# Kernel optimization log

Measured on AMD Instinct MI355X. Metric: run time of the kernel, lower is better.

The kernel has to match this reference:

```python
import jax, jax.numpy as jnp
import numpy as np
import math

B, S, D, H = 2, 2048, 2048, 16
HD = D // H            # 128
FF = 4 * D             # 8192
EPS = 1e-5


def _alibi_slopes(num_heads):
    # power-of-2 path (16 heads): slopes = base^i, base = 2^(-2^-(log2(n)-3))
    closest = 2 ** math.floor(math.log2(num_heads))
    base = 2.0 ** (-(2.0 ** (-(math.log2(closest) - 3))))
    powers = np.arange(1, 1 + closest, dtype=np.float32)
    slopes = base ** powers
    if closest != num_heads:
        extra_base = 2.0 ** (-(2.0 ** (-(math.log2(2 * closest) - 3))))
        num_rem = min(closest, num_heads - closest)
        extra_powers = np.arange(1, 1 + 2 * num_rem, 2, dtype=np.float32)
        slopes = np.concatenate([slopes, extra_base ** extra_powers])
    return jnp.asarray(slopes, dtype=jnp.float32)


def setup_inputs() -> dict:
    key = jax.random.key(0)
    ks = jax.random.split(key, 8)
    s = 0.02
    return {
        "x": jax.random.normal(ks[0], (B, S, D), dtype=jnp.float32),
        "ln1_w": jnp.ones((D,), jnp.float32),
        "ln1_b": jnp.zeros((D,), jnp.float32),
        "wqkv": jax.random.normal(ks[1], (D, 3 * D), jnp.float32) * s,
        "bqkv": jnp.zeros((3 * D,), jnp.float32),
        "wo": jax.random.normal(ks[2], (D, D), jnp.float32) * s,
        "bo": jnp.zeros((D,), jnp.float32),
        "ln2_w": jnp.ones((D,), jnp.float32),
        "ln2_b": jnp.zeros((D,), jnp.float32),
        "w1": jax.random.normal(ks[3], (D, FF), jnp.float32) * s,
        "b1": jnp.zeros((FF,), jnp.float32),
        "w2": jax.random.normal(ks[4], (FF, D), jnp.float32) * s,
        "b2": jnp.zeros((D,), jnp.float32),
    }


def _ln(x, w, b):
    mu = jnp.mean(x, axis=-1, keepdims=True)
    var = jnp.mean(jnp.square(x - mu), axis=-1, keepdims=True)
    return (x - mu) * jax.lax.rsqrt(var + EPS) * w + b


def reference(x, ln1_w, ln1_b, wqkv, bqkv, wo, bo, ln2_w, ln2_b, w1, b1, w2, b2):
    slopes = _alibi_slopes(H)                      # [H]
    # --- input layernorm + attention ---
    h = _ln(x, ln1_w, ln1_b)
    qkv = h @ wqkv + bqkv                          # [B,S,3D]
    q, k, v = jnp.split(qkv, 3, axis=-1)
    q = q.reshape(B, S, H, HD).transpose(0, 2, 1, 3)  # [B,H,S,HD]
    k = k.reshape(B, S, H, HD).transpose(0, 2, 1, 3)
    v = v.reshape(B, S, H, HD).transpose(0, 2, 1, 3)
    scores = jnp.einsum("bhqd,bhkd->bhqk", q, k) / math.sqrt(HD)
    pos = jnp.arange(S, dtype=jnp.float32)
    rel = pos[None, :] - pos[:, None]              # j - i
    alibi = slopes[:, None, None] * rel[None]      # [H,S,S]
    scores = scores.astype(jnp.float32) + alibi[None]
    causal = rel <= 0                              # j <= i
    scores = jnp.where(causal[None, None], scores, jnp.finfo(jnp.float32).min)
    probs = jax.nn.softmax(scores, axis=-1).astype(x.dtype)
    attn = jnp.einsum("bhqk,bhkd->bhqd", probs, v)  # [B,H,S,HD]
    attn = attn.transpose(0, 2, 1, 3).reshape(B, S, D)
    x = x + attn @ wo + bo
    # --- post-attn layernorm + GELU MLP ---
    h2 = _ln(x, ln2_w, ln2_b)
    m = jax.nn.gelu(h2 @ w1 + b1, approximate=True) @ w2 + b2
    return x + m
```

## Files before the change

kernel.cpp:

```cpp
#include <hip/hip_runtime.h>
#include <hip/hip_bf16.h>
#include <stdint.h>

#define BB 2
#define SS 2048
#define DD 2048
#define HH 16
#define HD 128
#define FFD 8192
#define TD (3*DD)

typedef unsigned short u16;
typedef __attribute__((ext_vector_type(8))) short s16x8;
typedef __attribute__((ext_vector_type(4))) float f32x4;

struct alignas(8) U16x4 { u16 a, b, c, d; };

__device__ __forceinline__ u16 f2b(float f) {
  union { float f; uint32_t u; } v; v.f = f;
  uint32_t r = (v.u + 0x7fffu + ((v.u >> 16) & 1u)) >> 16;
  return (u16)r;
}

__device__ __forceinline__ void async16(const void* g, void* l) {
  __builtin_amdgcn_global_load_lds((const __attribute__((address_space(1))) void*)g,
                                   (__attribute__((address_space(3))) void*)l,
                                   16, 0, 0);
}

__global__ __launch_bounds__(256) void wconv_t(const float* __restrict__ W,
                                               u16* __restrict__ Wt, int K, int N) {
  __shared__ float tile[64][65];
  int k0 = blockIdx.x * 64, n0 = blockIdx.y * 64;
  int c = threadIdx.x & 63, r0 = threadIdx.x >> 6;
#pragma unroll
  for (int i = 0; i < 16; ++i) {
    int r = i * 4 + r0;
    tile[r][c] = W[(size_t)(k0 + r) * N + n0 + c];
  }
  __syncthreads();
#pragma unroll
  for (int i = 0; i < 16; ++i) {
    int n = i * 4 + r0;
    Wt[(size_t)(n0 + n) * K + k0 + c] = f2b(tile[c][n]);
  }
}

__global__ __launch_bounds__(256) void ln_kernel(const float* __restrict__ X,
                                                 const float* __restrict__ g,
                                                 const float* __restrict__ be,
                                                 u16* __restrict__ O) {
  int row = blockIdx.x;
  const float* xr = X + (size_t)row * DD;
  int t = threadIdx.x;
  float4 v0 = ((const float4*)xr)[t];
  float4 v1 = ((const float4*)xr)[t + 256];
  float s = v0.x + v0.y + v0.z + v0.w + v1.x + v1.y + v1.z + v1.w;
  float q = v0.x*v0.x + v0.y*v0.y + v0.z*v0.z + v0.w*v0.w
          + v1.x*v1.x + v1.y*v1.y + v1.z*v1.z + v1.w*v1.w;
#pragma unroll
  for (int o = 32; o > 0; o >>= 1) { s += __shfl_down(s, o); q += __shfl_down(q, o); }
  __shared__ float red[8];
  if ((t & 63) == 0) { red[t >> 6] = s; red[4 + (t >> 6)] = q; }
  __syncthreads();
  float S = red[0] + red[1] + red[2] + red[3];
  float Q = red[4] + red[5] + red[6] + red[7];
  float mu = S * (1.0f / DD);
  float var = Q * (1.0f / DD) - mu * mu;
  float rs = rsqrtf(var + 1e-5f);
  float4 g0 = ((const float4*)g)[t],  g1 = ((const float4*)g)[t + 256];
  float4 b0 = ((const float4*)be)[t], b1 = ((const float4*)be)[t + 256];
  U16x4 o0, o1;
  o0.a = f2b((v0.x - mu) * rs * g0.x + b0.x);
  o0.b = f2b((v0.y - mu) * rs * g0.y + b0.y);
  o0.c = f2b((v0.z - mu) * rs * g0.z + b0.z);
  o0.d = f2b((v0.w - mu) * rs * g0.w + b0.w);
  o1.a = f2b((v1.x - mu) * rs * g1.x + b1.x);
  o1.b = f2b((v1.y - mu) * rs * g1.y + b1.y);
  o1.c = f2b((v1.z - mu) * rs * g1.z + b1.z);
  o1.d = f2b((v1.w - mu) * rs * g1.w + b1.w);
  *(U16x4*)(O + (size_t)row * DD + t * 4)         = o0;
  *(U16x4*)(O + (size_t)row * DD + (t + 256) * 4) = o1;
}

template <int MODE>
__global__ __launch_bounds__(256) void gemm_bt(const u16* __restrict__ A,
                                               const u16* __restrict__ Bt,
                                               const float* __restrict__ bias,
                                               const float* __restrict__ res,
                                               void* __restrict__ Cout,
                                               int M, int N, int K) {
  __shared__ __align__(16) u16 As[128 * 64];
  __shared__ __align__(16) u16 Bs[128 * 64];
  int n0 = blockIdx.x * 128, m0 = blockIdx.y * 128;
  int tid = threadIdx.x;
  int lane = tid & 63, w = tid >> 6;
  int wm = w >> 1, wn = w & 1;
  int col = lane & 15, quad = lane >> 4;
  f32x4 acc[4][4] = {};
  int arow = tid >> 3;
  int gkb = (tid & 7) ^ (arow & 7);
  const u16* ag = A  + (size_t)(m0 + arow) * K + gkb * 8;
  const u16* bg = Bt + (size_t)(n0 + arow) * K + gkb * 8;
  int sw = col & 7;
  for (int k0 = 0; k0 < K; k0 += 64) {
    __syncthreads();
#pragma unroll
    for (int s = 0; s < 4; ++s) {
      async16(ag + (size_t)s * 32 * K + k0, &As[s * 2048 + tid * 8]);
      async16(bg + (size_t)s * 32 * K + k0, &Bs[s * 2048 + tid * 8]);
    }
    __syncthreads();
#pragma unroll
    for (int kk = 0; kk < 64; kk += 32) {
      int kb = (kk >> 3) + quad;
      int slot = (kb ^ sw) * 8;
      s16x8 af[4], bf[4];
#pragma unroll
      for (int mt = 0; mt < 4; ++mt)
        af[mt] = *(const s16x8*)&As[(wm * 64 + mt * 16 + col) * 64 + slot];
#pragma unroll
      for (int nt = 0; nt < 4; ++nt)
        bf[nt] = *(const s16x8*)&Bs[(wn * 64 + nt * 16 + col) * 64 + slot];
#pragma unroll
      for (int mt = 0; mt < 4; ++mt)
#pragma unroll
        for (int nt = 0; nt < 4; ++nt)
          acc[mt][nt] = __builtin_amdgcn_mfma_f32_16x16x32_bf16(af[mt], bf[nt], acc[mt][nt], 0, 0, 0);
    }
  }
#pragma unroll
  for (int mt = 0; mt < 4; ++mt) {
    int mg = m0 + wm * 64 + mt * 16 + quad * 4;
#pragma unroll
    for (int nt = 0; nt < 4; ++nt) {
      int ng = n0 + wn * 64 + nt * 16 + col;
      float bn = bias[ng];
#pragma unroll
      for (int r = 0; r < 4; ++r) {
        float v = acc[mt][nt][r] + bn;
        size_t idx = (size_t)(mg + r) * N + ng;
        if (MODE == 1) {
          float u = 1.5957691216057308f * (v + 0.044715f * v * v * v);
          v = v / (1.0f + __expf(-u));
        }
        if (MODE == 2) {
          ((float*)Cout)[idx] = v + res[idx];
        } else {
          ((u16*)Cout)[idx] = f2b(v);
        }
      }
    }
  }
}

__global__ __launch_bounds__(256) void attn_kernel(const u16* __restrict__ qkv,
                                                   u16* __restrict__ out) {
  __shared__ __align__(16) u16 Ks[2][64 * 128];
  __shared__ __align__(16) u16 Vts[128 * 64];
  __shared__ __align__(16) u16 Ps[4][16 * 72];
  int bx = blockIdx.x, h = blockIdx.y, b = blockIdx.z;
  int tid = threadIdx.x, lane = tid & 63, w = tid >> 6;
  int col = lane & 15, quad = lane >> 4;
  const u16* base  = qkv + (size_t)b * SS * TD + (size_t)h * HD;
  const u16* kbase = base + DD;
  const u16* vbase = base + 2 * DD;
  float slope = exp2f(-0.5f * (float)(h + 1));
  const float scale = 0.088388347648318447f;
  int krow = tid >> 4;
  int ghb = (tid & 15) ^ (krow & 7);
  int vkey_loc = tid >> 4;
  int vhd0 = (tid & 15) * 8;
  int kxc = 8 * (tid & 7);

#pragma unroll 1
  for (int ph = 0; ph < 2; ++ph) {
    int qt = ph ? (31 - bx) : bx;
    int q0 = qt * 64;
    int ntile = qt + 1;
    int qr = q0 + w * 16 + col;
    s16x8 qf[4];
#pragma unroll
    for (int c = 0; c < 4; ++c)
      qf[c] = *(const s16x8*)(base + (size_t)qr * TD + c * 32 + quad * 8);
    float m_i[4] = {-1e30f, -1e30f, -1e30f, -1e30f};
    float l_i[4] = {0.f, 0.f, 0.f, 0.f};
    f32x4 oacc[8] = {};
#pragma unroll
    for (int s = 0; s < 4; ++s)
      async16(kbase + (size_t)(s * 16 + krow) * TD + ghb * 8,
              &Ks[0][s * 2048 + tid * 8]);
    s16x8 vreg[4];
#pragma unroll
    for (int s = 0; s < 4; ++s)
      vreg[s] = *(const s16x8*)(vbase + (size_t)(s * 16 + vkey_loc) * TD + vhd0);

    for (int t = 0; t < ntile; ++t) {
      int j0 = t * 64;
      __syncthreads();
      if (t + 1 < ntile) {
#pragma unroll
        for (int s = 0; s < 4; ++s)
          async16(kbase + (size_t)(j0 + 64 + s * 16 + krow) * TD + ghb * 8,
                  &Ks[(t + 1) & 1][s * 2048 + tid * 8]);
      }
#pragma unroll
      for (int s = 0; s < 4; ++s) {
        int key = s * 16 + vkey_loc;
#pragma unroll
        for (int j = 0; j < 8; ++j)
          Vts[(vhd0 + j) * 64 + (key ^ kxc)] = (u16)vreg[s][j];
      }
      if (t + 1 < ntile) {
#pragma unroll
        for (int s = 0; s < 4; ++s)
          vreg[s] = *(const s16x8*)(vbase + (size_t)(j0 + 64 + s * 16 + vkey_loc) * TD + vhd0);
      }
      const u16* kt_ = Ks[t & 1];
      f32x4 sc[4];
#pragma unroll
      for (int nt = 0; nt < 4; ++nt) {
        f32x4 s4 = {0.f, 0.f, 0.f, 0.f};
        int key = nt * 16 + col;
        int ksw = col & 7;
#pragma unroll
        for (int c = 0; c < 4; ++c) {
          s16x8 kf = *(const s16x8*)&kt_[key * 128 + (((c * 4 + quad) ^ ksw) * 8)];
          s4 = __builtin_amdgcn_mfma_f32_16x16x32_bf16(qf[c], kf, s4, 0, 0, 0);
        }
        sc[nt] = s4;
      }
      int rb = q0 + w * 16 + quad * 4;
      float p[4][4];
      float mt_[4] = {-1e30f, -1e30f, -1e30f, -1e30f};
#pragma unroll
      for (int nt = 0; nt < 4; ++nt) {
        int j = j0 + nt * 16 + col;
#pragma unroll
        for (int r = 0; r < 4; ++r) {
          float v = sc[nt][r] * scale + slope * (float)(j - (rb + r));
          if (j > rb + r) v = -1e30f;
          p[nt][r] = v;
          mt_[r] = fmaxf(mt_[r], v);
        }
      }
#pragma unroll
      for (int o = 1; o < 16; o <<= 1)
#pragma unroll
        for (int r = 0; r < 4; ++r) mt_[r] = fmaxf(mt_[r], __shfl_xor(mt_[r], o));
      float alpha[4];
#pragma unroll
      for (int r = 0; r < 4; ++r) {
        float mn = fmaxf(m_i[r], mt_[r]);
        alpha[r] = __expf(m_i[r] - mn);
        m_i[r] = mn;
      }
      float ls[4] = {0.f, 0.f, 0.f, 0.f};
#pragma unroll
      for (int nt = 0; nt < 4; ++nt)
#pragma unroll
        for (int r = 0; r < 4; ++r) {
          float e = __expf(p[nt][r] - m_i[r]);
          p[nt][r] = e;
          ls[r] += e;
        }
#pragma unroll
      for (int o = 1; o < 16; o <<= 1)
#pragma unroll
        for (int r = 0; r < 4; ++r) ls[r] += __shfl_xor(ls[r], o);
#pragma unroll
      for (int r = 0; r < 4; ++r) l_i[r] = l_i[r] * alpha[r] + ls[r];
#pragma unroll
      for (int ot = 0; ot < 8; ++ot)
#pragma unroll
        for (int r = 0; r < 4; ++r) oacc[ot][r] *= alpha[r];
#pragma unroll
      for (int nt = 0; nt < 4; ++nt)
#pragma unroll
        for (int r = 0; r < 4; ++r)
          Ps[w][(quad * 4 + r) * 72 + nt * 16 + col] = f2b(p[nt][r]);
      __syncthreads();
#pragma unroll
      for (int kt = 0; kt < 2; ++kt) {
        s16x8 pf = *(const s16x8*)&Ps[w][col * 72 + kt * 32 + quad * 8];
        int k8 = kt * 32 + quad * 8;
#pragma unroll
        for (int ot = 0; ot < 8; ++ot) {
          int hd = ot * 16 + col;
          int swz = 8 * ((hd >> 3) & 7);
          s16x8 vf = *(const s16x8*)&Vts[hd * 64 + (k8 ^ swz)];
          oacc[ot] = __builtin_amdgcn_mfma_f32_16x16x32_bf16(pf, vf, oacc[ot], 0, 0, 0);
        }
      }
    }
#pragma unroll
    for (int r = 0; r < 4; ++r) l_i[r] = 1.0f / l_i[r];
    u16* ob = out + ((size_t)b * SS + q0 + w * 16 + quad * 4) * DD + h * HD;
#pragma unroll
    for (int ot = 0; ot < 8; ++ot)
#pragma unroll
      for (int r = 0; r < 4; ++r)
        ob[(size_t)r * DD + ot * 16 + col] = f2b(oacc[ot][r] * l_i[r]);
  }
}

extern "C" void kernel_launch(void* const* d_in, const int* in_sizes, int n_in,
                              void* d_out, int out_size, void* d_ws, size_t ws_size,
                              hipStream_t stream) {
  const float* x    = (const float*)d_in[0];
  const float* ln1w = (const float*)d_in[1];
  const float* ln1b = (const float*)d_in[2];
  const float* wqkv = (const float*)d_in[3];
  const float* bqkv = (const float*)d_in[4];
  const float* wo   = (const float*)d_in[5];
  const float* bo   = (const float*)d_in[6];
  const float* ln2w = (const float*)d_in[7];
  const float* ln2b = (const float*)d_in[8];
  const float* w1   = (const float*)d_in[9];
  const float* b1   = (const float*)d_in[10];
  const float* w2   = (const float*)d_in[11];
  const float* b2   = (const float*)d_in[12];

  const int M = BB * SS;
  char* ws = (char*)d_ws;
  u16*  wt   = (u16*)ws;
  u16*  qkv  = (u16*)(ws + 33554432ull);
  u16*  cbuf = (u16*)(ws + 33554432ull + 50331648ull);
  float* r1  = (float*)(ws + 33554432ull + 50331648ull + 67108864ull);
  u16* h1 = cbuf;
  u16* attn = cbuf;
  u16* m1 = cbuf;
  u16* h2 = qkv;

  ln_kernel<<<M, 256, 0, stream>>>(x, ln1w, ln1b, h1);
  wconv_t<<<dim3(DD / 64, TD / 64), 256, 0, stream>>>(wqkv, wt, DD, TD);
  gemm_bt<0><<<dim3(TD / 128, M / 128), 256, 0, stream>>>(h1, wt, bqkv, nullptr, qkv, M, TD, DD);
  attn_kernel<<<dim3(16, HH, BB), 256, 0, stream>>>(qkv, attn);
  wconv_t<<<dim3(DD / 64, DD / 64), 256, 0, stream>>>(wo, wt, DD, DD);
  gemm_bt<2><<<dim3(DD / 128, M / 128), 256, 0, stream>>>(attn, wt, bo, x, r1, M, DD, DD);
  ln_kernel<<<M, 256, 0, stream>>>(r1, ln2w, ln2b, h2);
  wconv_t<<<dim3(DD / 64, FFD / 64), 256, 0, stream>>>(w1, wt, DD, FFD);
  gemm_bt<1><<<dim3(FFD / 128, M / 128), 256, 0, stream>>>(h2, wt, b1, nullptr, m1, M, FFD, DD);
  wconv_t<<<dim3(FFD / 64, DD / 64), 256, 0, stream>>>(w2, wt, FFD, DD);
  gemm_bt<2><<<dim3(DD / 128, M / 128), 256, 0, stream>>>(m1, wt, b2, r1, (float*)d_out, M, DD, FFD);
}
```

Measured before the change: 885.0 us.

## Replace GEMM with 8-wave 256x128 double-buffered pipelined kernel

The bf16 GEMM is replaced by an 8-wave (512-thread) kernel that computes a 256x128 output tile per block. Operand tiles are double-buffered in LDS, with the next K-tile's async loads issued while MFMAs run on the current buffer, and explicit vmcnt waits and s_barrier replace the two __syncthreads per iteration. It also uses s_setprio around the MFMA block and a new LDS swizzle for 32-wide K halves. The aim is to hide global-load latency and raise MFMA utilisation, at the cost of more LDS (two buffers) and fewer blocks in the grid.

```diff
diff --git a/kernel.cpp b/kernel.cpp
--- a/kernel.cpp
+++ b/kernel.cpp
@@ -84,51 +84,79 @@
 }
 
 template <int MODE>
-__global__ __launch_bounds__(256) void gemm_bt(const u16* __restrict__ A,
-                                               const u16* __restrict__ Bt,
-                                               const float* __restrict__ bias,
-                                               const float* __restrict__ res,
-                                               void* __restrict__ Cout,
-                                               int M, int N, int K) {
-  __shared__ __align__(16) u16 As[128 * 64];
-  __shared__ __align__(16) u16 Bs[128 * 64];
-  int n0 = blockIdx.x * 128, m0 = blockIdx.y * 128;
+__global__ __launch_bounds__(512, 2) void gemm8(const u16* __restrict__ A,
+                                                const u16* __restrict__ Bt,
+                                                const float* __restrict__ bias,
+                                                const float* __restrict__ res,
+                                                void* __restrict__ Cout,
+                                                int M, int N, int K) {
+  __shared__ __align__(16) u16 As[2][2][256 * 32];
+  __shared__ __align__(16) u16 Bs[2][2][128 * 32];
+
+  int n0 = blockIdx.x * 128, m0 = blockIdx.y * 256;
   int tid = threadIdx.x;
   int lane = tid & 63, w = tid >> 6;
-  int wm = w >> 1, wn = w & 1;
+  int wn = w & 1, wm = w >> 1;
   int col = lane & 15, quad = lane >> 4;
+
+  int r = tid >> 2, sl = tid & 3;
+  int gks = (sl ^ ((r >> 1) & 3)) * 8;
+  const u16* ag = A  + (size_t)(m0 + r) * K + gks;
+  const u16* bg = Bt + (size_t)(n0 + r) * K + gks;
+
+  int swz = (col >> 1) & 3;
+  int aoff = (wm * 64) * 32 + col * 32 + ((quad ^ swz) * 8);
+  int boff = (wn * 64) * 32 + col * 32 + ((quad ^ swz) * 8);
+
   f32x4 acc[4][4] = {};
-  int arow = tid >> 3;
-  int gkb = (tid & 7) ^ (arow & 7);
-  const u16* ag = A  + (size_t)(m0 + arow) * K + gkb * 8;
-  const u16* bg = Bt + (size_t)(n0 + arow) * K + gkb * 8;
-  int sw = col & 7;
-  for (int k0 = 0; k0 < K; k0 += 64) {
-    __syncthreads();
-#pragma unroll
-    for (int s = 0; s < 4; ++s) {
-      async16(ag + (size_t)s * 32 * K + k0, &As[s * 2048 + tid * 8]);
-      async16(bg + (size_t)s * 32 * K + k0, &Bs[s * 2048 + tid * 8]);
+  int ntiles = K >> 6;
+
+#pragma unroll
+  for (int kh = 0; kh < 2; ++kh) {
+    async16(ag + kh * 32, &As[0][kh][tid * 8]);
+    async16(ag + (size_t)128 * K + kh * 32, &As[0][kh][4096 + tid * 8]);
+    async16(bg + kh * 32, &Bs[0][kh][tid * 8]);
+  }
+  asm volatile("s_waitcnt vmcnt(0)" ::: "memory");
+  __builtin_amdgcn_s_barrier();
+
+  for (int t = 0; t < ntiles; ++t) {
+    int p = t & 1, pn = p ^ 1;
+    const u16* agn = ag + (t + 1) * 64;
+    const u16* bgn = bg + (t + 1) * 64;
+    bool pf = (t + 1 < ntiles);
+#pragma unroll
+    for (int kh = 0; kh < 2; ++kh) {
+      const u16* as_ = As[p][kh];
+      const u16* bs_ = Bs[p][kh];
+      s16x8 af[4], bf[4];
+#pragma unroll
+      for (int i = 0; i < 4; ++i)
+        bf[i] = *(const s16x8*)&bs_[boff + i * 512];
+#pragma unroll
+      for (int i = 0; i < 4; ++i)
+        af[i] = *(const s16x8*)&as_[aoff + i * 512];
+      if (pf) {
+        async16(agn + kh * 32, &As[pn][kh][tid * 8]);
+        async16(agn + (size_t)128 * K + kh * 32, &As[pn][kh][4096 + tid * 8]);
+        async16(bgn + kh * 32, &Bs[pn][kh][tid * 8]);
+        asm volatile("s_waitcnt vmcnt(3)" ::: "memory");
+      } else if (kh == 0) {
+        asm volatile("s_waitcnt vmcnt(0)" ::: "memory");
+      }
+      __builtin_amdgcn_s_barrier();
+      __builtin_amdgcn_s_setprio(1);
+#pragma unroll
+      for (int i = 0; i < 4; ++i)
+#pragma unroll
+        for (int j = 0; j < 4; ++j)
+          acc[i][j] = __builtin_amdgcn_mfma_f32_16x16x32_bf16(
+              af[i], bf[j], acc[i][j], 0, 0, 0);
+      __builtin_amdgcn_s_setprio(0);
+      __builtin_amdgcn_s_barrier();
     }
-    __syncthreads();
-#pragma unroll
-    for (int kk = 0; kk < 64; kk += 32) {
-      int kb = (kk >> 3) + quad;
-      int slot = (kb ^ sw) * 8;
-      s16x8 af[4], bf[4];
-#pragma unroll
-      for (int mt = 0; mt < 4; ++mt)
-        af[mt] = *(const s16x8*)&As[(wm * 64 + mt * 16 + col) * 64 + slot];
-#pragma unroll
-      for (int nt = 0; nt < 4; ++nt)
-        bf[nt] = *(const s16x8*)&Bs[(wn * 64 + nt * 16 + col) * 64 + slot];
-#pragma unroll
-      for (int mt = 0; mt < 4; ++mt)
-#pragma unroll
-        for (int nt = 0; nt < 4; ++nt)
-          acc[mt][nt] = __builtin_amdgcn_mfma_f32_16x16x32_bf16(af[mt], bf[nt], acc[mt][nt], 0, 0, 0);
-    }
-  }
+  }
+
 #pragma unroll
   for (int mt = 0; mt < 4; ++mt) {
     int mg = m0 + wm * 64 + mt * 16 + quad * 4;
@@ -137,9 +165,9 @@
       int ng = n0 + wn * 64 + nt * 16 + col;
       float bn = bias[ng];
 #pragma unroll
-      for (int r = 0; r < 4; ++r) {
-        float v = acc[mt][nt][r] + bn;
-        size_t idx = (size_t)(mg + r) * N + ng;
+      for (int rr = 0; rr < 4; ++rr) {
+        float v = acc[mt][nt][rr] + bn;
+        size_t idx = (size_t)(mg + rr) * N + ng;
         if (MODE == 1) {
           float u = 1.5957691216057308f * (v + 0.044715f * v * v * v);
           v = v / (1.0f + __expf(-u));
@@ -237,48 +265,48 @@
       for (int nt = 0; nt < 4; ++nt) {
         int j = j0 + nt * 16 + col;
 #pragma unroll
-        for (int r = 0; r < 4; ++r) {
-          float v = sc[nt][r] * scale + slope * (float)(j - (rb + r));
-          if (j > rb + r) v = -1e30f;
-          p[nt][r] = v;
-          mt_[r] = fmaxf(mt_[r], v);
+        for (int rr = 0; rr < 4; ++rr) {
+          float v = sc[nt][rr] * scale + slope * (float)(j - (rb + rr));
+          if (j > rb + rr) v = -1e30f;
+          p[nt][rr] = v;
+          mt_[rr] = fmaxf(mt_[rr], v);
         }
       }
 #pragma unroll
       for (int o = 1; o < 16; o <<= 1)
 #pragma unroll
-        for (int r = 0; r < 4; ++r) mt_[r] = fmaxf(mt_[r], __shfl_xor(mt_[r], o));
+        for (int rr = 0; rr < 4; ++rr) mt_[rr] = fmaxf(mt_[rr], __shfl_xor(mt_[rr], o));
       float alpha[4];
 #pragma unroll
-      for (int r = 0; r < 4; ++r) {
-        float mn = fmaxf(m_i[r], mt_[r]);
-        alpha[r] = __expf(m_i[r] - mn);
-        m_i[r] = mn;
+      for (int rr = 0; rr < 4; ++rr) {
+        float mn = fmaxf(m_i[rr], mt_[rr]);
+        alpha[rr] = __expf(m_i[rr] - mn);
+        m_i[rr] = mn;
       }
       float ls[4] = {0.f, 0.f, 0.f, 0.f};
 #pragma unroll
       for (int nt = 0; nt < 4; ++nt)
 #pragma unroll
-        for (int r = 0; r < 4; ++r) {
-          float e = __expf(p[nt][r] - m_i[r]);
-          p[nt][r] = e;
-          ls[r] += e;
+        for (int rr = 0; rr < 4; ++rr) {
+          float e = __expf(p[nt][rr] - m_i[rr]);
+          p[nt][rr] = e;
+          ls[rr] += e;
         }
 #pragma unroll
       for (int o = 1; o < 16; o <<= 1)
 #pragma unroll
-        for (int r = 0; r < 4; ++r) ls[r] += __shfl_xor(ls[r], o);
-#pragma unroll
-      for (int r = 0; r < 4; ++r) l_i[r] = l_i[r] * alpha[r] + ls[r];
+        for (int rr = 0; rr < 4; ++rr) ls[rr] += __shfl_xor(ls[rr], o);
+#pragma unroll
+      for (int rr = 0; rr < 4; ++rr) l_i[rr] = l_i[rr] * alpha[rr] + ls[rr];
 #pragma unroll
       for (int ot = 0; ot < 8; ++ot)
 #pragma unroll
-        for (int r = 0; r < 4; ++r) oacc[ot][r] *= alpha[r];
+        for (int rr = 0; rr < 4; ++rr) oacc[ot][rr] *= alpha[rr];
 #pragma unroll
       for (int nt = 0; nt < 4; ++nt)
 #pragma unroll
-        for (int r = 0; r < 4; ++r)
-          Ps[w][(quad * 4 + r) * 72 + nt * 16 + col] = f2b(p[nt][r]);
+        for (int rr = 0; rr < 4; ++rr)
+          Ps[w][(quad * 4 + rr) * 72 + nt * 16 + col] = f2b(p[nt][rr]);
       __syncthreads();
 #pragma unroll
       for (int kt = 0; kt < 2; ++kt) {
@@ -294,13 +322,13 @@
       }
     }
 #pragma unroll
-    for (int r = 0; r < 4; ++r) l_i[r] = 1.0f / l_i[r];
+    for (int rr = 0; rr < 4; ++rr) l_i[rr] = 1.0f / l_i[rr];
     u16* ob = out + ((size_t)b * SS + q0 + w * 16 + quad * 4) * DD + h * HD;
 #pragma unroll
     for (int ot = 0; ot < 8; ++ot)
 #pragma unroll
-      for (int r = 0; r < 4; ++r)
-        ob[(size_t)r * DD + ot * 16 + col] = f2b(oacc[ot][r] * l_i[r]);
+      for (int rr = 0; rr < 4; ++rr)
+        ob[(size_t)rr * DD + ot * 16 + col] = f2b(oacc[ot][rr] * l_i[rr]);
   }
 }
 
@@ -334,13 +362,13 @@
 
   ln_kernel<<<M, 256, 0, stream>>>(x, ln1w, ln1b, h1);
   wconv_t<<<dim3(DD / 64, TD / 64), 256, 0, stream>>>(wqkv, wt, DD, TD);
-  gemm_bt<0><<<dim3(TD / 128, M / 128), 256, 0, stream>>>(h1, wt, bqkv, nullptr, qkv, M, TD, DD);
+  gemm8<0><<<dim3(TD / 128, M / 256), 512, 0, stream>>>(h1, wt, bqkv, nullptr, qkv, M, TD, DD);
   attn_kernel<<<dim3(16, HH, BB), 256, 0, stream>>>(qkv, attn);
   wconv_t<<<dim3(DD / 64, DD / 64), 256, 0, stream>>>(wo, wt, DD, DD);
-  gemm_bt<2><<<dim3(DD / 128, M / 128), 256, 0, stream>>>(attn, wt, bo, x, r1, M, DD, DD);
+  gemm8<2><<<dim3(DD / 128, M / 256), 512, 0, stream>>>(attn, wt, bo, x, r1, M, DD, DD);
   ln_kernel<<<M, 256, 0, stream>>>(r1, ln2w, ln2b, h2);
   wconv_t<<<dim3(DD / 64, FFD / 64), 256, 0, stream>>>(w1, wt, DD, FFD);
-  gemm_bt<1><<<dim3(FFD / 128, M / 128), 256, 0, stream>>>(h2, wt, b1, nullptr, m1, M, FFD, DD);
+  gemm8<1><<<dim3(FFD / 128, M / 256), 512, 0, stream>>>(h2, wt, b1, nullptr, m1, M, FFD, DD);
   wconv_t<<<dim3(FFD / 64, DD / 64), 256, 0, stream>>>(w2, wt, FFD, DD);
-  gemm_bt<2><<<dim3(DD / 128, M / 128), 256, 0, stream>>>(m1, wt, b2, r1, (float*)d_out, M, DD, FFD);
-}
+  gemm8<2><<<dim3(DD / 128, M / 256), 512, 0, stream>>>(m1, wt, b2, r1, (float*)d_out, M, DD, FFD);
+}
```

Measured after the change: 912.5 us. 1.03x slower.
